# Kernel tuning notes

Hardware: AMD Instinct MI355X
Metric: run time of the kernel (lower is better)

## Reference

```python
import jax, jax.numpy as jnp
import numpy as np

B, D, L, G, K, U, OUT = 131072, 256, 3, 4, 128, 64, 10


def setup_inputs() -> dict:
    key = jax.random.key(0)
    k1, k2, k3, k4 = jax.random.split(key, 4)
    x = jax.random.normal(k1, (B, D), dtype=jnp.float32)
    # per-level, per-group input node coords into the previous level's output
    idx = jax.random.randint(k2, (L, G, K), 0, D, dtype=jnp.int32)
    # per-group kernels [fan_in, units] and biases [units], stacked
    W = jax.random.normal(k3, (L, G, K, U), dtype=jnp.float32) * 0.1
    b = jnp.zeros((L, G, U), dtype=jnp.float32)
    W_out = jax.random.normal(k4, (D, OUT), dtype=jnp.float32) * 0.1
    b_out = jnp.zeros((OUT,), dtype=jnp.float32)
    return {"x": x, "idx": idx, "W": W, "b": b, "W_out": W_out, "b_out": b_out}


def reference(x, idx, W, b, W_out, b_out):
    # Each topological level: for every dependency-group g, gather K scalar
    # columns from the previous level (the per-node slice+concat in the
    # original), tiny matmul [B,K]@[K,U] + bias, tanh; level output is the
    # concat of group outputs -> [B, G*U]. Groups share shapes, so they are
    # batched over axis g with a single einsum per level.
    h = x
    n_levels = W.shape[0]
    for l in range(n_levels):  # small fixed loop over topology levels
        gathered = h[:, idx[l]]                                  # [B, G, K]
        z = jnp.einsum('bgk,gku->bgu', gathered, W[l]) + b[l]    # [B, G, U]
        h = jnp.tanh(z).reshape(z.shape[0], -1)                  # [B, G*U]
    # output level: single group fed by all previous nodes, linear out activation
    return h @ W_out + b_out                                      # [B, OUT]
```

## Files before the change

kernel.cpp:

```cpp
#include <hip/hip_runtime.h>

typedef unsigned short ushort_t;
typedef __attribute__((ext_vector_type(8))) short short8;
typedef __attribute__((ext_vector_type(4))) float floatx4;

#define DD 256
#define LL 3
#define GG 4
#define KK 128
#define UU 64
#define OUTN 10
#define HSTRIDE 264
#define MROWS 128
#define NT 2

__device__ __forceinline__ ushort_t f2bf(float f) {
  unsigned u = __builtin_bit_cast(unsigned, f);
  u = (u + 0x7FFFu + ((u >> 16) & 1u)) >> 16;
  return (ushort_t)u;
}

__device__ __forceinline__ unsigned pack_bf2(float lo, float hi) {
  unsigned a = __builtin_bit_cast(unsigned, hi) + 0x8000u;
  unsigned b = __builtin_bit_cast(unsigned, lo) + 0x8000u;
  return __builtin_amdgcn_perm(a, b, 0x07060302u);
}

__device__ __forceinline__ float fast_tanh(float x) {
  float e = __builtin_amdgcn_exp2f(x * 2.885390081777927f);
  return __builtin_fmaf(-2.0f, __builtin_amdgcn_rcpf(e + 1.0f), 1.0f);
}

__global__ __launch_bounds__(256) void prep_kernel(
    const int* __restrict__ idx, const float* __restrict__ W,
    const float* __restrict__ Wout, ushort_t* __restrict__ AT,
    ushort_t* __restrict__ WoT) {
  int b = blockIdx.x;
  int t = threadIdx.x;
  if (b < LL * DD) {
    int l = b >> 8, n = b & 255, g = n >> 6, u = n & 63;
    __shared__ int sidx[KK];
    __shared__ float sw[KK];
    if (t < KK) {
      sidx[t] = idx[(l * GG + g) * KK + t];
      sw[t]   = W[((size_t)((l * GG + g) * KK + t)) * UU + u];
    }
    __syncthreads();
    float s = 0.f;
#pragma unroll 8
    for (int j = 0; j < KK; j++) s += (sidx[j] == t) ? sw[j] : 0.f;
    AT[(b << 8) | t] = f2bf(s);
  } else {
    int e2 = (b - LL * DD) * 256 + t;
    int n = e2 >> 8, k = e2 & 255;
    WoT[e2] = (n < OUTN) ? f2bf(Wout[k * OUTN + n]) : (ushort_t)0;
  }
}

__global__ __launch_bounds__(512, 4) void fused_kernel(
    const float* __restrict__ x, const float* __restrict__ bias,
    const float* __restrict__ bout, const ushort_t* __restrict__ AT,
    const ushort_t* __restrict__ WoT, float* __restrict__ out) {
  __shared__ ushort_t hbuf[MROWS * HSTRIDE];

  const int tid  = threadIdx.x;
  const int wave = tid >> 6;
  const int lane = tid & 63;
  const int quad = lane >> 4;
  const int l16  = lane & 15;
  const long row0 = (long)blockIdx.x * MROWS;

  const float4* xv = (const float4*)(x + row0 * DD);
#pragma unroll
  for (int i = 0; i < 16; i++) {
    int f  = tid + i * 512;
    int r  = f >> 6;
    int c4 = f & 63;
    float4 v = xv[r * 64 + c4];
    uint2 w;
    w.x = pack_bf2(v.x, v.y);
    w.y = pack_bf2(v.z, v.w);
    *(uint2*)&hbuf[r * HSTRIDE + c4 * 4] = w;
  }
  __syncthreads();

#pragma unroll 1
  for (int l = 0; l < 3; l++) {
    const ushort_t* Ab = AT + l * (DD * DD) + (wave * 32 + l16) * DD + quad * 8;
    const ushort_t* hsrc = hbuf + l16 * HSTRIDE + quad * 8;

    floatx4 acc[8][NT];
#pragma unroll
    for (int nt = 0; nt < NT; nt++) {
      float4 bv = *(const float4*)&bias[l * DD + wave * 32 + nt * 16 + quad * 4];
      floatx4 ini = {bv.x, bv.y, bv.z, bv.w};
#pragma unroll
      for (int mt = 0; mt < 8; mt++) acc[mt][nt] = ini;
    }

    short8 wf[NT], wfn[NT];
#pragma unroll
    for (int nt = 0; nt < NT; nt++) wf[nt] = *(const short8*)&Ab[nt * 16 * DD];

#pragma unroll
    for (int ks = 0; ks < 8; ks++) {
      if (ks < 7) {
#pragma unroll
        for (int nt = 0; nt < NT; nt++)
          wfn[nt] = *(const short8*)&Ab[nt * 16 * DD + (ks + 1) * 32];
      }
      short8 bfc = *(const short8*)&hsrc[0 * 16 * HSTRIDE + ks * 32];
#pragma unroll
      for (int mt = 0; mt < 8; mt++) {
        short8 bfn;
        if (mt < 7) bfn = *(const short8*)&hsrc[(mt + 1) * 16 * HSTRIDE + ks * 32];
        acc[mt][0] = __builtin_amdgcn_mfma_f32_16x16x32_bf16(wf[0], bfc, acc[mt][0], 0, 0, 0);
        acc[mt][1] = __builtin_amdgcn_mfma_f32_16x16x32_bf16(wf[1], bfc, acc[mt][1], 0, 0, 0);
        bfc = bfn;
      }
#pragma unroll
      for (int nt = 0; nt < NT; nt++) wf[nt] = wfn[nt];
    }
    __syncthreads();

#pragma unroll
    for (int nt = 0; nt < NT; nt++) {
#pragma unroll
      for (int mt = 0; mt < 8; mt++) {
        uint2 w;
        w.x = pack_bf2(fast_tanh(acc[mt][nt][0]), fast_tanh(acc[mt][nt][1]));
        w.y = pack_bf2(fast_tanh(acc[mt][nt][2]), fast_tanh(acc[mt][nt][3]));
        *(uint2*)&hbuf[(mt * 16 + l16) * HSTRIDE + wave * 32 + nt * 16 + quad * 4] = w;
      }
    }
    __syncthreads();
  }

  short8 wof[8];
#pragma unroll
  for (int ks = 0; ks < 8; ks++)
    wof[ks] = *(const short8*)&WoT[l16 * DD + ks * 32 + quad * 8];

  floatx4 accf = {0.f, 0.f, 0.f, 0.f};
#pragma unroll
  for (int ks = 0; ks < 8; ks++) {
    short8 bfr = *(const short8*)&hbuf[(wave * 16 + l16) * HSTRIDE + ks * 32 + quad * 8];
    accf = __builtin_amdgcn_mfma_f32_16x16x32_bf16(wof[ks], bfr, accf, 0, 0, 0);
  }
  const long obase = (row0 + wave * 16 + l16) * OUTN;
  if (quad < 2) {
    float4 p = {accf[0] + bout[quad * 4 + 0], accf[1] + bout[quad * 4 + 1],
                accf[2] + bout[quad * 4 + 2], accf[3] + bout[quad * 4 + 3]};
    *(float4*)&out[obase + quad * 4] = p;
  } else if (quad == 2) {
    float2 p = {accf[0] + bout[8], accf[1] + bout[9]};
    *(float2*)&out[obase + 8] = p;
  }
}

extern "C" void kernel_launch(void* const* d_in, const int* in_sizes, int n_in,
                              void* d_out, int out_size, void* d_ws, size_t ws_size,
                              hipStream_t stream) {
  const float* x    = (const float*)d_in[0];
  const int*   idx  = (const int*)d_in[1];
  const float* W    = (const float*)d_in[2];
  const float* b    = (const float*)d_in[3];
  const float* Wout = (const float*)d_in[4];
  const float* bout = (const float*)d_in[5];
  float* out = (float*)d_out;

  ushort_t* AT  = (ushort_t*)d_ws;
  ushort_t* WoT = AT + LL * DD * DD;

  prep_kernel<<<LL * DD + 16, 256, 0, stream>>>(idx, W, Wout, AT, WoT);
  fused_kernel<<<131072 / MROWS, 512, 0, stream>>>(x, b, bout, AT, WoT, out);
}
```

Before: 257.4 us.

## Shrink row tile to 32 with 2x2 wave layout over outputs

Reduces rows per block from 128 to 32 and threads to 256, arranging four waves as 2 row-tiles by 2 column halves so each wave computes 16 rows by 128 outputs. This cuts LDS use per block and raises occupancy and block count to hide latency. In exchange, each weight fragment loaded from global memory is reused across only one M tile instead of eight, greatly increasing L2 weight traffic, and the output stage uses only half the waves.

```diff
diff --git a/kernel.cpp b/kernel.cpp
--- a/kernel.cpp
+++ b/kernel.cpp
@@ -11,8 +11,7 @@
 #define UU 64
 #define OUTN 10
 #define HSTRIDE 264
-#define MROWS 128
-#define NT 2
+#define MROWS 32
 
 __device__ __forceinline__ ushort_t f2bf(float f) {
   unsigned u = __builtin_bit_cast(unsigned, f);
@@ -57,7 +56,7 @@
   }
 }
 
-__global__ __launch_bounds__(512, 4) void fused_kernel(
+__global__ __launch_bounds__(256, 5) void fused_kernel(
     const float* __restrict__ x, const float* __restrict__ bias,
     const float* __restrict__ bout, const ushort_t* __restrict__ AT,
     const ushort_t* __restrict__ WoT, float* __restrict__ out) {
@@ -68,12 +67,14 @@
   const int lane = tid & 63;
   const int quad = lane >> 4;
   const int l16  = lane & 15;
+  const int wm   = wave >> 1;
+  const int wn   = wave & 1;
   const long row0 = (long)blockIdx.x * MROWS;
 
   const float4* xv = (const float4*)(x + row0 * DD);
 #pragma unroll
-  for (int i = 0; i < 16; i++) {
-    int f  = tid + i * 512;
+  for (int i = 0; i < 8; i++) {
+    int f  = tid + i * 256;
     int r  = f >> 6;
     int c4 = f & 63;
     float4 v = xv[r * 64 + c4];
@@ -86,75 +87,64 @@
 
 #pragma unroll 1
   for (int l = 0; l < 3; l++) {
-    const ushort_t* Ab = AT + l * (DD * DD) + (wave * 32 + l16) * DD + quad * 8;
-    const ushort_t* hsrc = hbuf + l16 * HSTRIDE + quad * 8;
+    const ushort_t* Ab   = AT + l * (DD * DD) + (wn * 128 + l16) * DD + quad * 8;
+    const ushort_t* hsrc = hbuf + (wm * 16 + l16) * HSTRIDE + quad * 8;
 
-    floatx4 acc[8][NT];
+    floatx4 acc[8];
 #pragma unroll
-    for (int nt = 0; nt < NT; nt++) {
-      float4 bv = *(const float4*)&bias[l * DD + wave * 32 + nt * 16 + quad * 4];
+    for (int nt = 0; nt < 8; nt++) {
+      float4 bv = *(const float4*)&bias[l * DD + wn * 128 + nt * 16 + quad * 4];
       floatx4 ini = {bv.x, bv.y, bv.z, bv.w};
-#pragma unroll
-      for (int mt = 0; mt < 8; mt++) acc[mt][nt] = ini;
+      acc[nt] = ini;
     }
 
-    short8 wf[NT], wfn[NT];
-#pragma unroll
-    for (int nt = 0; nt < NT; nt++) wf[nt] = *(const short8*)&Ab[nt * 16 * DD];
-
+    short8 bf = *(const short8*)&hsrc[0];
 #pragma unroll
     for (int ks = 0; ks < 8; ks++) {
-      if (ks < 7) {
+      short8 af[8];
 #pragma unroll
-        for (int nt = 0; nt < NT; nt++)
-          wfn[nt] = *(const short8*)&Ab[nt * 16 * DD + (ks + 1) * 32];
-      }
-      short8 bfc = *(const short8*)&hsrc[0 * 16 * HSTRIDE + ks * 32];
+      for (int nt = 0; nt < 8; nt++)
+        af[nt] = *(const short8*)&Ab[nt * 16 * DD + ks * 32];
+      short8 bfn;
+      if (ks < 7) bfn = *(const short8*)&hsrc[(ks + 1) * 32];
 #pragma unroll
-      for (int mt = 0; mt < 8; mt++) {
-        short8 bfn;
-        if (mt < 7) bfn = *(const short8*)&hsrc[(mt + 1) * 16 * HSTRIDE + ks * 32];
-        acc[mt][0] = __builtin_amdgcn_mfma_f32_16x16x32_bf16(wf[0], bfc, acc[mt][0], 0, 0, 0);
-        acc[mt][1] = __builtin_amdgcn_mfma_f32_16x16x32_bf16(wf[1], bfc, acc[mt][1], 0, 0, 0);
-        bfc = bfn;
-      }
-#pragma unroll
-      for (int nt = 0; nt < NT; nt++) wf[nt] = wfn[nt];
+      for (int nt = 0; nt < 8; nt++)
+        acc[nt] = __builtin_amdgcn_mfma_f32_16x16x32_bf16(af[nt], bf, acc[nt], 0, 0, 0);
+      bf = bfn;
     }
     __syncthreads();
 
 #pragma unroll
-    for (int nt = 0; nt < NT; nt++) {
-#pragma unroll
-      for (int mt = 0; mt < 8; mt++) {
-        uint2 w;
-        w.x = pack_bf2(fast_tanh(acc[mt][nt][0]), fast_tanh(acc[mt][nt][1]));
-        w.y = pack_bf2(fast_tanh(acc[mt][nt][2]), fast_tanh(acc[mt][nt][3]));
-        *(uint2*)&hbuf[(mt * 16 + l16) * HSTRIDE + wave * 32 + nt * 16 + quad * 4] = w;
-      }
+    for (int nt = 0; nt < 8; nt++) {
+      uint2 w;
+      w.x = pack_bf2(fast_tanh(acc[nt][0]), fast_tanh(acc[nt][1]));
+      w.y = pack_bf2(fast_tanh(acc[nt][2]), fast_tanh(acc[nt][3]));
+      *(uint2*)&hbuf[(wm * 16 + l16) * HSTRIDE + wn * 128 + nt * 16 + quad * 4] = w;
     }
     __syncthreads();
   }
 
-  short8 wof[8];
+  if (wave < 2) {
+    short8 wof[8];
 #pragma unroll
-  for (int ks = 0; ks < 8; ks++)
-    wof[ks] = *(const short8*)&WoT[l16 * DD + ks * 32 + quad * 8];
+    for (int ks = 0; ks < 8; ks++)
+      wof[ks] = *(const short8*)&WoT[l16 * DD + ks * 32 + quad * 8];
 
-  floatx4 accf = {0.f, 0.f, 0.f, 0.f};
+    floatx4 accf = {0.f, 0.f, 0.f, 0.f};
 #pragma unroll
-  for (int ks = 0; ks < 8; ks++) {
-    short8 bfr = *(const short8*)&hbuf[(wave * 16 + l16) * HSTRIDE + ks * 32 + quad * 8];
-    accf = __builtin_amdgcn_mfma_f32_16x16x32_bf16(wof[ks], bfr, accf, 0, 0, 0);
-  }
-  const long obase = (row0 + wave * 16 + l16) * OUTN;
-  if (quad < 2) {
-    float4 p = {accf[0] + bout[quad * 4 + 0], accf[1] + bout[quad * 4 + 1],
-                accf[2] + bout[quad * 4 + 2], accf[3] + bout[quad * 4 + 3]};
-    *(float4*)&out[obase + quad * 4] = p;
-  } else if (quad == 2) {
-    float2 p = {accf[0] + bout[8], accf[1] + bout[9]};
-    *(float2*)&out[obase + 8] = p;
+    for (int ks = 0; ks < 8; ks++) {
+      short8 bfr = *(const short8*)&hbuf[(wave * 16 + l16) * HSTRIDE + ks * 32 + quad * 8];
+      accf = __builtin_amdgcn_mfma_f32_16x16x32_bf16(wof[ks], bfr, accf, 0, 0, 0);
+    }
+    const long obase = (row0 + wave * 16 + l16) * OUTN;
+    if (quad < 2) {
+      float4 p = {accf[0] + bout[quad * 4 + 0], accf[1] + bout[quad * 4 + 1],
+                  accf[2] + bout[quad * 4 + 2], accf[3] + bout[quad * 4 + 3]};
+      *(float4*)&out[obase + quad * 4] = p;
+    } else if (quad == 2) {
+      float2 p = {accf[0] + bout[8], accf[1] + bout[9]};
+      *(float2*)&out[obase + 8] = p;
+    }
   }
 }
 
@@ -173,5 +163,5 @@
   ushort_t* WoT = AT + LL * DD * DD;
 
   prep_kernel<<<LL * DD + 16, 256, 0, stream>>>(idx, W, Wout, AT, WoT);
-  fused_kernel<<<131072 / MROWS, 512, 0, stream>>>(x, b, bout, AT, WoT, out);
+  fused_kernel<<<131072 / MROWS, 256, 0, stream>>>(x, b, bout, AT, WoT, out);
 }
```

New measurement: 552.9 us. 115% more time.

## Halve rows per block and double-buffer LDS activations to drop a barrier

Applied to the files above, without the earlier changes.

Each block now handles 64 rows instead of 128, so the accumulator tile shrinks from 8x2 to 4x2 per wave and register pressure drops. The activation buffer in LDS is ping-ponged between two halves, which removes the barrier that separated the MFMA reads from the tanh writes in each level. The inner loop now prefetches all four B fragments and both A fragments for the next k-step. In exchange the grid doubles, so the AT weights are reloaded from global/L2 for half as many rows per block. Only half the waves do the final output projection.

```diff
diff --git a/kernel.cpp b/kernel.cpp
--- a/kernel.cpp
+++ b/kernel.cpp
@@ -11,8 +11,7 @@
 #define UU 64
 #define OUTN 10
 #define HSTRIDE 264
-#define MROWS 128
-#define NT 2
+#define MROWS 64
 
 __device__ __forceinline__ ushort_t f2bf(float f) {
   unsigned u = __builtin_bit_cast(unsigned, f);
@@ -61,7 +60,7 @@
     const float* __restrict__ x, const float* __restrict__ bias,
     const float* __restrict__ bout, const ushort_t* __restrict__ AT,
     const ushort_t* __restrict__ WoT, float* __restrict__ out) {
-  __shared__ ushort_t hbuf[MROWS * HSTRIDE];
+  __shared__ ushort_t hbuf[2][MROWS * HSTRIDE];
 
   const int tid  = threadIdx.x;
   const int wave = tid >> 6;
@@ -72,7 +71,7 @@
 
   const float4* xv = (const float4*)(x + row0 * DD);
 #pragma unroll
-  for (int i = 0; i < 16; i++) {
+  for (int i = 0; i < 8; i++) {
     int f  = tid + i * 512;
     int r  = f >> 6;
     int c4 = f & 63;
@@ -80,81 +79,90 @@
     uint2 w;
     w.x = pack_bf2(v.x, v.y);
     w.y = pack_bf2(v.z, v.w);
-    *(uint2*)&hbuf[r * HSTRIDE + c4 * 4] = w;
+    *(uint2*)&hbuf[0][r * HSTRIDE + c4 * 4] = w;
   }
   __syncthreads();
 
 #pragma unroll 1
   for (int l = 0; l < 3; l++) {
+    const int pr = l & 1, pw = pr ^ 1;
     const ushort_t* Ab = AT + l * (DD * DD) + (wave * 32 + l16) * DD + quad * 8;
-    const ushort_t* hsrc = hbuf + l16 * HSTRIDE + quad * 8;
+    const ushort_t* hs = hbuf[pr] + l16 * HSTRIDE + quad * 8;
 
-    floatx4 acc[8][NT];
+    floatx4 acc[4][2];
 #pragma unroll
-    for (int nt = 0; nt < NT; nt++) {
+    for (int nt = 0; nt < 2; nt++) {
       float4 bv = *(const float4*)&bias[l * DD + wave * 32 + nt * 16 + quad * 4];
       floatx4 ini = {bv.x, bv.y, bv.z, bv.w};
 #pragma unroll
-      for (int mt = 0; mt < 8; mt++) acc[mt][nt] = ini;
+      for (int mt = 0; mt < 4; mt++) acc[mt][nt] = ini;
     }
 
-    short8 wf[NT], wfn[NT];
-#pragma unroll
-    for (int nt = 0; nt < NT; nt++) wf[nt] = *(const short8*)&Ab[nt * 16 * DD];
+    short8 a0 = *(const short8*)&Ab[0];
+    short8 a1 = *(const short8*)&Ab[16 * DD];
+    short8 b0 = *(const short8*)&hs[0 * 16 * HSTRIDE];
+    short8 b1 = *(const short8*)&hs[1 * 16 * HSTRIDE];
+    short8 b2 = *(const short8*)&hs[2 * 16 * HSTRIDE];
+    short8 b3 = *(const short8*)&hs[3 * 16 * HSTRIDE];
 
 #pragma unroll
     for (int ks = 0; ks < 8; ks++) {
+      short8 na0, na1, nb0, nb1, nb2, nb3;
       if (ks < 7) {
-#pragma unroll
-        for (int nt = 0; nt < NT; nt++)
-          wfn[nt] = *(const short8*)&Ab[nt * 16 * DD + (ks + 1) * 32];
+        const int o = (ks + 1) * 32;
+        nb0 = *(const short8*)&hs[0 * 16 * HSTRIDE + o];
+        nb1 = *(const short8*)&hs[1 * 16 * HSTRIDE + o];
+        nb2 = *(const short8*)&hs[2 * 16 * HSTRIDE + o];
+        nb3 = *(const short8*)&hs[3 * 16 * HSTRIDE + o];
+        na0 = *(const short8*)&Ab[o];
+        na1 = *(const short8*)&Ab[16 * DD + o];
       }
-      short8 bfc = *(const short8*)&hsrc[0 * 16 * HSTRIDE + ks * 32];
-#pragma unroll
-      for (int mt = 0; mt < 8; mt++) {
-        short8 bfn;
-        if (mt < 7) bfn = *(const short8*)&hsrc[(mt + 1) * 16 * HSTRIDE + ks * 32];
-        acc[mt][0] = __builtin_amdgcn_mfma_f32_16x16x32_bf16(wf[0], bfc, acc[mt][0], 0, 0, 0);
-        acc[mt][1] = __builtin_amdgcn_mfma_f32_16x16x32_bf16(wf[1], bfc, acc[mt][1], 0, 0, 0);
-        bfc = bfn;
-      }
-#pragma unroll
-      for (int nt = 0; nt < NT; nt++) wf[nt] = wfn[nt];
+      acc[0][0] = __builtin_amdgcn_mfma_f32_16x16x32_bf16(a0, b0, acc[0][0], 0, 0, 0);
+      acc[0][1] = __builtin_amdgcn_mfma_f32_16x16x32_bf16(a1, b0, acc[0][1], 0, 0, 0);
+      acc[1][0] = __builtin_amdgcn_mfma_f32_16x16x32_bf16(a0, b1, acc[1][0], 0, 0, 0);
+      acc[1][1] = __builtin_amdgcn_mfma_f32_16x16x32_bf16(a1, b1, acc[1][1], 0, 0, 0);
+      acc[2][0] = __builtin_amdgcn_mfma_f32_16x16x32_bf16(a0, b2, acc[2][0], 0, 0, 0);
+      acc[2][1] = __builtin_amdgcn_mfma_f32_16x16x32_bf16(a1, b2, acc[2][1], 0, 0, 0);
+      acc[3][0] = __builtin_amdgcn_mfma_f32_16x16x32_bf16(a0, b3, acc[3][0], 0, 0, 0);
+      acc[3][1] = __builtin_amdgcn_mfma_f32_16x16x32_bf16(a1, b3, acc[3][1], 0, 0, 0);
+      a0 = na0; a1 = na1;
+      b0 = nb0; b1 = nb1; b2 = nb2; b3 = nb3;
     }
-    __syncthreads();
 
 #pragma unroll
-    for (int nt = 0; nt < NT; nt++) {
+    for (int mt = 0; mt < 4; mt++) {
 #pragma unroll
-      for (int mt = 0; mt < 8; mt++) {
+      for (int nt = 0; nt < 2; nt++) {
         uint2 w;
         w.x = pack_bf2(fast_tanh(acc[mt][nt][0]), fast_tanh(acc[mt][nt][1]));
         w.y = pack_bf2(fast_tanh(acc[mt][nt][2]), fast_tanh(acc[mt][nt][3]));
-        *(uint2*)&hbuf[(mt * 16 + l16) * HSTRIDE + wave * 32 + nt * 16 + quad * 4] = w;
+        *(uint2*)&hbuf[pw][(mt * 16 + l16) * HSTRIDE + wave * 32 + nt * 16 + quad * 4] = w;
       }
     }
     __syncthreads();
   }
 
-  short8 wof[8];
+  if (wave < 4) {
+    short8 wof[8];
 #pragma unroll
-  for (int ks = 0; ks < 8; ks++)
-    wof[ks] = *(const short8*)&WoT[l16 * DD + ks * 32 + quad * 8];
+    for (int ks = 0; ks < 8; ks++)
+      wof[ks] = *(const short8*)&WoT[l16 * DD + ks * 32 + quad * 8];
 
-  floatx4 accf = {0.f, 0.f, 0.f, 0.f};
+    floatx4 accf = {0.f, 0.f, 0.f, 0.f};
 #pragma unroll
-  for (int ks = 0; ks < 8; ks++) {
-    short8 bfr = *(const short8*)&hbuf[(wave * 16 + l16) * HSTRIDE + ks * 32 + quad * 8];
-    accf = __builtin_amdgcn_mfma_f32_16x16x32_bf16(wof[ks], bfr, accf, 0, 0, 0);
-  }
-  const long obase = (row0 + wave * 16 + l16) * OUTN;
-  if (quad < 2) {
-    float4 p = {accf[0] + bout[quad * 4 + 0], accf[1] + bout[quad * 4 + 1],
-                accf[2] + bout[quad * 4 + 2], accf[3] + bout[quad * 4 + 3]};
-    *(float4*)&out[obase + quad * 4] = p;
-  } else if (quad == 2) {
-    float2 p = {accf[0] + bout[8], accf[1] + bout[9]};
-    *(float2*)&out[obase + 8] = p;
+    for (int ks = 0; ks < 8; ks++) {
+      short8 bfr = *(const short8*)&hbuf[1][(wave * 16 + l16) * HSTRIDE + ks * 32 + quad * 8];
+      accf = __builtin_amdgcn_mfma_f32_16x16x32_bf16(wof[ks], bfr, accf, 0, 0, 0);
+    }
+    const long obase = (row0 + wave * 16 + l16) * OUTN;
+    if (quad < 2) {
+      float4 p = {accf[0] + bout[quad * 4 + 0], accf[1] + bout[quad * 4 + 1],
+                  accf[2] + bout[quad * 4 + 2], accf[3] + bout[quad * 4 + 3]};
+      *(float4*)&out[obase + quad * 4] = p;
+    } else if (quad == 2) {
+      float2 p = {accf[0] + bout[8], accf[1] + bout[9]};
+      *(float2*)&out[obase + 8] = p;
+    }
   }
 }
 
```

After: 289.4 us. 1.12x slower.

## Shrink row tile to 64 and preload full weight fragments per wave

Applied to the files above, without the earlier changes.

Each block now handles 64 rows with 4 waves instead of 128 rows with 8 waves. Each wave makes two passes over 32-column output slices and loads all eight K-step weight fragments into registers up front. Activation fragments from LDS are double-buffered across row tiles. The aim is to raise per-wave MFMA density and overlap LDS reads with MFMA issue. In exchange, L2 reads of the weight matrix per output row double, and register pressure rises, with the launch bound relaxed to compensate.

```diff
diff --git a/kernel.cpp b/kernel.cpp
--- a/kernel.cpp
+++ b/kernel.cpp
@@ -11,8 +11,7 @@
 #define UU 64
 #define OUTN 10
 #define HSTRIDE 264
-#define MROWS 128
-#define NT 2
+#define MROWS 64
 
 __device__ __forceinline__ ushort_t f2bf(float f) {
   unsigned u = __builtin_bit_cast(unsigned, f);
@@ -57,7 +56,7 @@
   }
 }
 
-__global__ __launch_bounds__(512, 4) void fused_kernel(
+__global__ __launch_bounds__(256, 2) void fused_kernel(
     const float* __restrict__ x, const float* __restrict__ bias,
     const float* __restrict__ bout, const ushort_t* __restrict__ AT,
     const ushort_t* __restrict__ WoT, float* __restrict__ out) {
@@ -73,7 +72,7 @@
   const float4* xv = (const float4*)(x + row0 * DD);
 #pragma unroll
   for (int i = 0; i < 16; i++) {
-    int f  = tid + i * 512;
+    int f  = tid + i * 256;
     int r  = f >> 6;
     int c4 = f & 63;
     float4 v = xv[r * 64 + c4];
@@ -84,53 +83,62 @@
   }
   __syncthreads();
 
+  const ushort_t* hsrc = hbuf + l16 * HSTRIDE + quad * 8;
+
 #pragma unroll 1
   for (int l = 0; l < 3; l++) {
-    const ushort_t* Ab = AT + l * (DD * DD) + (wave * 32 + l16) * DD + quad * 8;
-    const ushort_t* hsrc = hbuf + l16 * HSTRIDE + quad * 8;
-
-    floatx4 acc[8][NT];
+    floatx4 acc[2][4][2];
 #pragma unroll
-    for (int nt = 0; nt < NT; nt++) {
-      float4 bv = *(const float4*)&bias[l * DD + wave * 32 + nt * 16 + quad * 4];
-      floatx4 ini = {bv.x, bv.y, bv.z, bv.w};
+    for (int p = 0; p < 2; p++) {
 #pragma unroll
-      for (int mt = 0; mt < 8; mt++) acc[mt][nt] = ini;
+      for (int nt = 0; nt < 2; nt++) {
+        float4 bv = *(const float4*)&bias[l * DD + p * 128 + wave * 32 + nt * 16 + quad * 4];
+        floatx4 ini = {bv.x, bv.y, bv.z, bv.w};
+#pragma unroll
+        for (int mt = 0; mt < 4; mt++) acc[p][mt][nt] = ini;
+      }
     }
 
-    short8 wf[NT], wfn[NT];
 #pragma unroll
-    for (int nt = 0; nt < NT; nt++) wf[nt] = *(const short8*)&Ab[nt * 16 * DD];
-
+    for (int p = 0; p < 2; p++) {
+      const ushort_t* Ab = AT + l * (DD * DD) + (p * 128 + wave * 32 + l16) * DD + quad * 8;
+      short8 a0[8], a1[8];
 #pragma unroll
-    for (int ks = 0; ks < 8; ks++) {
-      if (ks < 7) {
+      for (int ks = 0; ks < 8; ks++) {
+        a0[ks] = *(const short8*)&Ab[ks * 32];
+        a1[ks] = *(const short8*)&Ab[16 * DD + ks * 32];
+      }
+      short8 b[2][8];
 #pragma unroll
-        for (int nt = 0; nt < NT; nt++)
-          wfn[nt] = *(const short8*)&Ab[nt * 16 * DD + (ks + 1) * 32];
+      for (int ks = 0; ks < 8; ks++) b[0][ks] = *(const short8*)&hsrc[ks * 32];
+#pragma unroll
+      for (int mt = 0; mt < 4; mt++) {
+        const int cb = mt & 1, nb = cb ^ 1;
+        if (mt < 3) {
+#pragma unroll
+          for (int ks = 0; ks < 8; ks++)
+            b[nb][ks] = *(const short8*)&hsrc[(mt + 1) * 16 * HSTRIDE + ks * 32];
+        }
+#pragma unroll
+        for (int ks = 0; ks < 8; ks++) {
+          acc[p][mt][0] = __builtin_amdgcn_mfma_f32_16x16x32_bf16(a0[ks], b[cb][ks], acc[p][mt][0], 0, 0, 0);
+          acc[p][mt][1] = __builtin_amdgcn_mfma_f32_16x16x32_bf16(a1[ks], b[cb][ks], acc[p][mt][1], 0, 0, 0);
+        }
       }
-      short8 bfc = *(const short8*)&hsrc[0 * 16 * HSTRIDE + ks * 32];
-#pragma unroll
-      for (int mt = 0; mt < 8; mt++) {
-        short8 bfn;
-        if (mt < 7) bfn = *(const short8*)&hsrc[(mt + 1) * 16 * HSTRIDE + ks * 32];
-        acc[mt][0] = __builtin_amdgcn_mfma_f32_16x16x32_bf16(wf[0], bfc, acc[mt][0], 0, 0, 0);
-        acc[mt][1] = __builtin_amdgcn_mfma_f32_16x16x32_bf16(wf[1], bfc, acc[mt][1], 0, 0, 0);
-        bfc = bfn;
-      }
-#pragma unroll
-      for (int nt = 0; nt < NT; nt++) wf[nt] = wfn[nt];
     }
     __syncthreads();
 
 #pragma unroll
-    for (int nt = 0; nt < NT; nt++) {
+    for (int p = 0; p < 2; p++) {
 #pragma unroll
-      for (int mt = 0; mt < 8; mt++) {
-        uint2 w;
-        w.x = pack_bf2(fast_tanh(acc[mt][nt][0]), fast_tanh(acc[mt][nt][1]));
-        w.y = pack_bf2(fast_tanh(acc[mt][nt][2]), fast_tanh(acc[mt][nt][3]));
-        *(uint2*)&hbuf[(mt * 16 + l16) * HSTRIDE + wave * 32 + nt * 16 + quad * 4] = w;
+      for (int mt = 0; mt < 4; mt++) {
+#pragma unroll
+        for (int nt = 0; nt < 2; nt++) {
+          uint2 w;
+          w.x = pack_bf2(fast_tanh(acc[p][mt][nt][0]), fast_tanh(acc[p][mt][nt][1]));
+          w.y = pack_bf2(fast_tanh(acc[p][mt][nt][2]), fast_tanh(acc[p][mt][nt][3]));
+          *(uint2*)&hbuf[(mt * 16 + l16) * HSTRIDE + p * 128 + wave * 32 + nt * 16 + quad * 4] = w;
+        }
       }
     }
     __syncthreads();
@@ -173,5 +181,5 @@
   ushort_t* WoT = AT + LL * DD * DD;
 
   prep_kernel<<<LL * DD + 16, 256, 0, stream>>>(idx, W, Wout, AT, WoT);
-  fused_kernel<<<131072 / MROWS, 512, 0, stream>>>(x, b, bout, AT, WoT, out);
+  fused_kernel<<<131072 / MROWS, 256, 0, stream>>>(x, b, bout, AT, WoT, out);
 }
```

After: 306.2 us. 1.19x slower.
